# Performance work log

Hardware: AMD Instinct MI355X
Metric: run time of the kernel (lower is better)

## Reference

```python
import jax, jax.numpy as jnp
import numpy as np

HEADS = 8
DIM_HEAD = 96
INNER = HEADS * DIM_HEAD  # 768
PEP_DIM = 768
PRO_DIM = 768
SCALE = DIM_HEAD ** -0.5
NEG = -1000000.0
EPS = 1e-5


def _layer_norm(x, g, b):
    mu = jnp.mean(x, axis=-1, keepdims=True)
    var = jnp.mean(jnp.square(x - mu), axis=-1, keepdims=True)
    return (x - mu) * jax.lax.rsqrt(var + EPS) * g + b


def setup_inputs() -> dict:
    key = jax.random.key(0)
    ks = jax.random.split(key, 12)
    b, n, m = 16, 128, 2048
    peptide = jax.random.normal(ks[0], (b, n, PEP_DIM), dtype=jnp.float32)
    protein = jax.random.normal(ks[1], (b, m, PRO_DIM), dtype=jnp.float32)
    peptide_mask = jax.random.randint(ks[2], (b, n), 0, 2, dtype=jnp.int32)
    pro_mask = jax.random.randint(ks[3], (b, m), 0, 2, dtype=jnp.int32)
    s = 0.02
    Wq = jax.random.normal(ks[4], (PEP_DIM, INNER), dtype=jnp.float32) * s
    Wk = jax.random.normal(ks[5], (PRO_DIM, INNER), dtype=jnp.float32) * s
    Wv_prot = jax.random.normal(ks[6], (PRO_DIM, INNER), dtype=jnp.float32) * s
    Wv_pep = jax.random.normal(ks[7], (PEP_DIM, INNER), dtype=jnp.float32) * s
    Wo_prot = jax.random.normal(ks[8], (INNER, PEP_DIM), dtype=jnp.float32) * s
    bo_prot = jnp.zeros((PEP_DIM,), dtype=jnp.float32)
    Wo_pep = jax.random.normal(ks[9], (INNER, PRO_DIM), dtype=jnp.float32) * s
    bo_pep = jnp.zeros((PRO_DIM,), dtype=jnp.float32)
    ln_g = jnp.ones((PEP_DIM,), dtype=jnp.float32)
    ln_b = jnp.zeros((PEP_DIM,), dtype=jnp.float32)
    return {
        'peptide': peptide, 'protein': protein,
        'peptide_mask': peptide_mask, 'pro_mask': pro_mask,
        'Wq': Wq, 'Wk': Wk, 'Wv_prot': Wv_prot, 'Wv_pep': Wv_pep,
        'Wo_prot': Wo_prot, 'bo_prot': bo_prot,
        'Wo_pep': Wo_pep, 'bo_pep': bo_pep,
        'ln_g': ln_g, 'ln_b': ln_b,
    }


def reference(peptide, protein, peptide_mask, pro_mask,
              Wq, Wk, Wv_prot, Wv_pep, Wo_prot, bo_prot, Wo_pep, bo_pep,
              ln_g, ln_b):
    b, n, _ = peptide.shape
    m = protein.shape[1]
    # projections -> (b, h, len, d)
    q = (peptide @ Wq).reshape(b, n, HEADS, DIM_HEAD).transpose(0, 2, 1, 3)
    k = (protein @ Wk).reshape(b, m, HEADS, DIM_HEAD).transpose(0, 2, 1, 3)
    v_prot = (protein @ Wv_prot).reshape(b, m, HEADS, DIM_HEAD).transpose(0, 2, 1, 3)
    v_pep = (peptide @ Wv_pep).reshape(b, n, HEADS, DIM_HEAD).transpose(0, 2, 1, 3)
    # scores (b, h, n, m)
    dots = jnp.einsum('bhnd,bhmd->bhnm', q, k) * SCALE
    dots = jnp.where(peptide_mask[:, None, :, None] == 0, NEG, dots)
    dots = jnp.where(pro_mask[:, None, None, :] == 0, NEG, dots)
    attn = jax.nn.softmax(dots, axis=-1)
    # peptide-side output: rows of attn aggregate protein values
    out_protein = jnp.einsum('bhnm,bhmd->bhnd', attn, v_prot)
    out_protein = out_protein.transpose(0, 2, 1, 3).reshape(b, n, INNER)
    out_protein = out_protein @ Wo_prot + bo_prot
    out_protein = _layer_norm(out_protein + peptide, ln_g, ln_b)
    # protein-side output: attn^T aggregates peptide values
    out_peptide = jnp.einsum('bhnm,bhnd->bhmd', attn, v_pep)
    out_peptide = out_peptide.transpose(0, 2, 1, 3).reshape(b, m, INNER)
    out_peptide = out_peptide @ Wo_pep + bo_pep
    out_peptide = _layer_norm(out_peptide + protein, ln_g, ln_b)
    return (out_protein, out_peptide, attn)
```

## Files before the change

### kernel.cpp

```cpp
#include <hip/hip_runtime.h>
#include <math.h>

static constexpr int HEADS  = 8;
static constexpr int DHEAD  = 96;
static constexpr int INNER  = 768;
static constexpr int NPEP   = 128;
static constexpr int MPRO   = 2048;
static constexpr float ATT_SCALE = 0.10206207261596577f;
static constexpr float NEGF   = -1000000.0f;
static constexpr float LN_EPS = 1e-5f;

typedef __attribute__((ext_vector_type(8))) short bf16x8;
typedef __attribute__((ext_vector_type(4))) float f32x4;

__device__ __forceinline__ unsigned short f2b(float f) {
    unsigned u = __builtin_bit_cast(unsigned, f);
    u += 0x7fffu + ((u >> 16) & 1u);
    return (unsigned short)(u >> 16);
}
__device__ __forceinline__ float b2f(unsigned short u) {
    return __builtin_bit_cast(float, (unsigned)u << 16);
}

__device__ __forceinline__ void async16(const unsigned short* g, unsigned short* l) {
    __builtin_amdgcn_global_load_lds(
        (const __attribute__((address_space(1))) void*)g,
        (__attribute__((address_space(3))) void*)l, 16, 0, 0);
}

template<int TM, int MODE>
__global__ __launch_bounds__(256) void gemm_bf16(
    const unsigned short* __restrict__ A, const unsigned short* __restrict__ B,
    unsigned short* __restrict__ C,
    int M, int N, int K, int lda, int ldb, int ldc,
    long sAb, long sAh, long sBb, long sBh, long sCb, long sCh,
    int lenShift, int nxSwz,
    const unsigned short* __restrict__ B2, unsigned short* __restrict__ C2)
{
    (void)M;
    constexpr int FR   = TM / 32;
    constexpr int PIPE = 3;
    __shared__ unsigned short As[PIPE][TM * 32];
    __shared__ unsigned short Bs[PIPE][128 * 32];

    const int tid = threadIdx.x;
    int bx, by;
    if (nxSwz > 0) {
        const int bid = blockIdx.x;
        const int per = gridDim.x >> 3;
        const int v   = (bid & 7) * per + (bid >> 3);
        bx = v % nxSwz; by = v / nxSwz;
    } else { bx = blockIdx.x; by = blockIdx.y; }
    int n0        = bx * 128;
    const int m0  = by * TM;
    const int z   = blockIdx.z;
    const int zb  = z >> 3, zh = z & 7;

    bool sideB = false;
    if (MODE == 5 && n0 >= 768) { sideB = true; n0 -= 768; }

    const unsigned short* Ab = A + zb * sAb + zh * sAh;
    const unsigned short* Bb = ((MODE == 5 && sideB) ? B2 : B) + zb * sBb + zh * sBh;

    const int rS = tid >> 2;
    const int kS = (((tid & 3) ^ ((rS >> 1) & 3)) * 8);
    const int wave = tid >> 6;

    const int lane = tid & 63;
    const int l16  = lane & 15;
    const int quad = lane >> 4;
    const int wr   = (wave >> 1) * (TM / 2);
    const int wc   = (wave & 1) * 64;

    f32x4 acc[FR][4];
#pragma unroll
    for (int i = 0; i < FR; ++i)
#pragma unroll
        for (int j = 0; j < 4; ++j) acc[i][j] = (f32x4){0.f, 0.f, 0.f, 0.f};

    auto stageT = [&](int t, int bi) {
        const int k0 = t << 5;
        unsigned short* a0 = &As[bi][wave * 512];
        async16(Ab + (long)(m0 + rS) * lda + k0 + kS, a0);
        if (TM == 128)
            async16(Ab + (long)(m0 + 64 + rS) * lda + k0 + kS, a0 + 2048);
        int bR0 = n0 + rS;      if (bR0 > N - 1) bR0 = N - 1;
        int bR1 = n0 + 64 + rS; if (bR1 > N - 1) bR1 = N - 1;
        unsigned short* b0 = &Bs[bi][wave * 512];
        async16(Bb + (long)bR0 * ldb + k0 + kS, b0);
        async16(Bb + (long)bR1 * ldb + k0 + kS, b0 + 2048);
    };

    const int NT = K >> 5;
    stageT(0, 0);
    if (NT > 1) stageT(1, 1);
    if (NT > 2) stageT(2, 2);

    int bi = 0;
    for (int t = 0; t < NT; ++t) {
        const int ahead = NT - 1 - t;
        if constexpr (TM == 128) {
            if (ahead >= 2)      asm volatile("s_waitcnt vmcnt(8)" ::: "memory");
            else if (ahead == 1) asm volatile("s_waitcnt vmcnt(4)" ::: "memory");
            else                 asm volatile("s_waitcnt vmcnt(0)" ::: "memory");
        } else {
            if (ahead >= 2)      asm volatile("s_waitcnt vmcnt(6)" ::: "memory");
            else if (ahead == 1) asm volatile("s_waitcnt vmcnt(3)" ::: "memory");
            else                 asm volatile("s_waitcnt vmcnt(0)" ::: "memory");
        }
        __builtin_amdgcn_s_barrier();

        bf16x8 af[FR], bfr[4];
#pragma unroll
        for (int i = 0; i < FR; ++i) {
            const int rA = wr + i * 16 + l16;
            af[i] = *reinterpret_cast<const bf16x8*>(
                &As[bi][rA * 32 + ((quad ^ ((rA >> 1) & 3)) * 8)]);
        }
#pragma unroll
        for (int j = 0; j < 4; ++j) {
            const int rB = wc + j * 16 + l16;
            bfr[j] = *reinterpret_cast<const bf16x8*>(
                &Bs[bi][rB * 32 + ((quad ^ ((rB >> 1) & 3)) * 8)]);
        }

        __builtin_amdgcn_s_setprio(1);
#pragma unroll
        for (int i = 0; i < FR; ++i)
#pragma unroll
            for (int j = 0; j < 4; ++j)
                acc[i][j] = __builtin_amdgcn_mfma_f32_16x16x32_bf16(af[i], bfr[j], acc[i][j], 0, 0, 0);
        __builtin_amdgcn_s_setprio(0);

        __builtin_amdgcn_s_barrier();
        __builtin_amdgcn_sched_barrier(0);
        if (t + PIPE < NT) stageT(t + PIPE, bi);
        bi = bi + 1; if (bi == PIPE) bi = 0;
    }

#pragma unroll
    for (int i = 0; i < FR; ++i) {
#pragma unroll
        for (int j = 0; j < 4; ++j) {
            const int col = n0 + wc + j * 16 + l16;
            if ((MODE == 2) && col >= N) continue;
            const int h = col / 96, d = col - h * 96;
#pragma unroll
            for (int r = 0; r < 4; ++r) {
                const int row = m0 + wr + i * 16 + quad * 4 + r;
                float v = acc[i][j][r];
                if (MODE == 1) {
                    v *= ATT_SCALE;
                    C[zb * sCb + zh * sCh + (long)row * ldc + col] = f2b(v);
                } else if (MODE == 2) {
                    C[zb * sCb + zh * sCh + (long)row * ldc + col] = f2b(v);
                } else if (MODE == 3) {
                    const int bb = row >> lenShift, rr = row & ((1 << lenShift) - 1);
                    C[(((long)(bb * 8 + h) << lenShift) + rr) * 96 + d] = f2b(v);
                } else if (MODE == 4) {
                    const int bb = row >> lenShift, rr = row & ((1 << lenShift) - 1);
                    C[(((long)(bb * 8 + h) * 96 + d) << lenShift) + rr] = f2b(v);
                } else {
                    const int bb = row >> lenShift, rr = row & ((1 << lenShift) - 1);
                    if (!sideB)
                        C [(((long)(bb * 8 + h) << lenShift) + rr) * 96 + d] = f2b(v);
                    else
                        C2[(((long)(bb * 8 + h) * 96 + d) << lenShift) + rr] = f2b(v);
                }
            }
        }
    }
}

__global__ __launch_bounds__(256) void fusedpv_kernel(
    const unsigned short* __restrict__ attn16,
    const unsigned short* __restrict__ vprotT,
    const unsigned short* __restrict__ vpepT,
    unsigned short* __restrict__ opp,
    unsigned short* __restrict__ opep)
{
    __shared__ unsigned short AttT[128 * 136];
    __shared__ unsigned short Vp[96 * 136];

    const int id = blockIdx.x;
    const int z  = ((id >> 4) << 3) + (id & 7);
    const int nh = (id >> 3) & 1;
    const int b  = z >> 3, h = z & 7;

    const unsigned short* Az = attn16 + (long)z * NPEP * MPRO;
    const unsigned short* Vz = vprotT + (long)z * 96 * MPRO;
    const unsigned short* Pz = vpepT  + (long)z * 96 * 128;

    const int tid  = threadIdx.x;
    const int lane = tid & 63;
    const int l16  = lane & 15;
    const int quad = lane >> 4;
    const int wave = tid >> 6;
    const int wrN  = (wave >> 1) * 32;
    const int wrM  = (wave >> 1) * 64;
    const int wcD  = (wave & 1) * 48;

#pragma unroll
    for (int e = 0; e < 6; ++e) {
        const int c = tid + e * 256;
        const int row = c >> 4, coloff = (c & 15) * 8;
        bf16x8 v = *reinterpret_cast<const bf16x8*>(Pz + row * 128 + coloff);
        *reinterpret_cast<bf16x8*>(&Vp[row * 136 + coloff]) = v;
    }
    __syncthreads();

    f32x4 acc1[2][3];
#pragma unroll
    for (int i = 0; i < 2; ++i)
#pragma unroll
        for (int j = 0; j < 3; ++j) acc1[i][j] = (f32x4){0.f, 0.f, 0.f, 0.f};

    for (int cc = 0; cc < 16; ++cc) {
        const int m0 = cc * 128;
        const bool own = (cc >> 3) == nh;

        bf16x8 a1[2][4], b1[3][4];
#pragma unroll
        for (int i = 0; i < 2; ++i) {
            const int n = nh * 64 + wrN + i * 16 + l16;
#pragma unroll
            for (int kc = 0; kc < 4; ++kc)
                a1[i][kc] = *reinterpret_cast<const bf16x8*>(
                    Az + (long)n * MPRO + m0 + kc * 32 + quad * 8);
        }
#pragma unroll
        for (int j = 0; j < 3; ++j) {
            const int d = wcD + j * 16 + l16;
#pragma unroll
            for (int kc = 0; kc < 4; ++kc)
                b1[j][kc] = *reinterpret_cast<const bf16x8*>(
                    Vz + (long)d * MPRO + m0 + kc * 32 + quad * 8);
        }

        if (own) {
            const int mBase = (tid & 7) * 16;
#pragma unroll
            for (int nn = 0; nn < 128; nn += 32) {
                const int n = nn + (tid >> 3);
#pragma unroll
                for (int c = 0; c < 2; ++c) {
                    bf16x8 v = *reinterpret_cast<const bf16x8*>(
                        Az + (long)n * MPRO + m0 + mBase + c * 8);
#pragma unroll
                    for (int jj = 0; jj < 8; ++jj)
                        AttT[(mBase + c * 8 + jj) * 136 + n] = (unsigned short)v[jj];
                }
            }
            __syncthreads();
        }

#pragma unroll
        for (int kc = 0; kc < 4; ++kc)
#pragma unroll
            for (int i = 0; i < 2; ++i)
#pragma unroll
                for (int j = 0; j < 3; ++j)
                    acc1[i][j] = __builtin_amdgcn_mfma_f32_16x16x32_bf16(
                        a1[i][kc], b1[j][kc], acc1[i][j], 0, 0, 0);

        if (own) {
            f32x4 acc2[4][3];
#pragma unroll
            for (int i = 0; i < 4; ++i)
#pragma unroll
                for (int j = 0; j < 3; ++j) acc2[i][j] = (f32x4){0.f, 0.f, 0.f, 0.f};
#pragma unroll
            for (int kc = 0; kc < 4; ++kc) {
                bf16x8 a2[4], b2v[3];
#pragma unroll
                for (int i = 0; i < 4; ++i)
                    a2[i] = *reinterpret_cast<const bf16x8*>(
                        &AttT[(wrM + i * 16 + l16) * 136 + kc * 32 + quad * 8]);
#pragma unroll
                for (int j = 0; j < 3; ++j)
                    b2v[j] = *reinterpret_cast<const bf16x8*>(
                        &Vp[(wcD + j * 16 + l16) * 136 + kc * 32 + quad * 8]);
#pragma unroll
                for (int i = 0; i < 4; ++i)
#pragma unroll
                    for (int j = 0; j < 3; ++j)
                        acc2[i][j] = __builtin_amdgcn_mfma_f32_16x16x32_bf16(
                            a2[i], b2v[j], acc2[i][j], 0, 0, 0);
            }
#pragma unroll
            for (int i = 0; i < 4; ++i)
#pragma unroll
                for (int j = 0; j < 3; ++j) {
                    const int d = wcD + j * 16 + l16;
#pragma unroll
                    for (int r = 0; r < 4; ++r) {
                        const int m = m0 + wrM + i * 16 + quad * 4 + r;
                        opep[(long)b * MPRO * INNER + (long)m * INNER + h * 96 + d]
                            = f2b(acc2[i][j][r]);
                    }
                }
            __syncthreads();
        }
    }

#pragma unroll
    for (int i = 0; i < 2; ++i)
#pragma unroll
        for (int j = 0; j < 3; ++j) {
            const int d = wcD + j * 16 + l16;
#pragma unroll
            for (int r = 0; r < 4; ++r) {
                const int n = nh * 64 + wrN + i * 16 + quad * 4 + r;
                opp[((long)b * NPEP + n) * INNER + h * 96 + d] = f2b(acc1[i][j][r]);
            }
        }
}

__global__ __launch_bounds__(256) void conv2_kernel(
    const float* __restrict__ pro, const float* __restrict__ pep,
    unsigned short* __restrict__ pro16, unsigned short* __restrict__ pep16,
    int nPro4, int nPep4)
{
    const int i = blockIdx.x * 256 + threadIdx.x;
    const float* in; unsigned short* out; int idx;
    if (i < nPro4) { in = pro; out = pro16; idx = i; }
    else { idx = i - nPro4; if (idx >= nPep4) return; in = pep; out = pep16; }
    float4 v = reinterpret_cast<const float4*>(in)[idx];
    ushort4 o;
    o.x = f2b(v.x); o.y = f2b(v.y); o.z = f2b(v.z); o.w = f2b(v.w);
    reinterpret_cast<ushort4*>(out)[idx] = o;
}

__global__ __launch_bounds__(256) void wtrans_kernel(
    const float* w0, const float* w1, const float* w2,
    const float* w3, const float* w4, const float* w5,
    unsigned short* o0, unsigned short* o1, unsigned short* o2,
    unsigned short* o3, unsigned short* o4, unsigned short* o5)
{
    const float* in; unsigned short* out;
    switch (blockIdx.z) {
        case 0: in = w0; out = o0; break;
        case 1: in = w1; out = o1; break;
        case 2: in = w2; out = o2; break;
        case 3: in = w3; out = o3; break;
        case 4: in = w4; out = o4; break;
        default: in = w5; out = o5; break;
    }
    __shared__ unsigned short t[32][33];
    const int bx = blockIdx.x * 32, by = blockIdx.y * 32;
    const int x = threadIdx.x, y = threadIdx.y;
#pragma unroll
    for (int i = 0; i < 32; i += 8)
        t[y + i][x] = f2b(in[(long)(by + y + i) * 768 + bx + x]);
    __syncthreads();
#pragma unroll
    for (int i = 0; i < 32; i += 8)
        out[(long)(bx + y + i) * 768 + by + x] = t[x][y + i];
}

__global__ __launch_bounds__(256) void softmax_kernel(
    unsigned short* __restrict__ s16, float* __restrict__ attn,
    const int* __restrict__ pepm, const int* __restrict__ prom)
{
    __shared__ float smx[4], sms[4];
    const long row = blockIdx.x;
    const int b = (int)(row >> 10);
    const int n = (int)(row & 127);
    unsigned short* p16 = s16 + row * (long)MPRO;
    float* pf = attn + row * (long)MPRO;
    const int tid = threadIdx.x;
    const int wv = tid >> 6;
    const int rowOk = pepm[(b << 7) + n];

    float v[8];
    float mx = -3.4e38f;
    if (rowOk) {
#pragma unroll
        for (int k = 0; k < 8; ++k) {
            const int c = tid + k * 256;
            float x = b2f(p16[c]);
            if (prom[(b << 11) + c] == 0) x = NEGF;
            v[k] = x; mx = fmaxf(mx, x);
        }
    } else {
#pragma unroll
        for (int k = 0; k < 8; ++k) v[k] = NEGF;
        mx = NEGF;
    }
#pragma unroll
    for (int off = 32; off > 0; off >>= 1) mx = fmaxf(mx, __shfl_xor(mx, off));
    if ((tid & 63) == 0) smx[wv] = mx;
    __syncthreads();
    mx = fmaxf(fmaxf(smx[0], smx[1]), fmaxf(smx[2], smx[3]));

    float sum = 0.f;
#pragma unroll
    for (int k = 0; k < 8; ++k) { v[k] = __expf(v[k] - mx); sum += v[k]; }
#pragma unroll
    for (int off = 32; off > 0; off >>= 1) sum += __shfl_xor(sum, off);
    if ((tid & 63) == 0) sms[wv] = sum;
    __syncthreads();
    const float inv = 1.0f / (sms[0] + sms[1] + sms[2] + sms[3]);
#pragma unroll
    for (int k = 0; k < 8; ++k) {
        const float o = v[k] * inv;
        pf[tid + k * 256] = o;
        p16[tid + k * 256] = f2b(o);
    }
}

__global__ __launch_bounds__(256) void bias_res_ln(
    const unsigned short* __restrict__ tmp, const float* __restrict__ bias,
    const float* __restrict__ res, const float* __restrict__ gam,
    const float* __restrict__ bet, float* __restrict__ out)
{
    __shared__ float red[8];
    const long row = blockIdx.x;
    const unsigned short* t = tmp + row * INNER;
    const float* r = res + row * INNER;
    float* o = out + row * INNER;
    const int tid = threadIdx.x;
    const int wv = tid >> 6;

    float v[3]; float s = 0.f;
#pragma unroll
    for (int k = 0; k < 3; ++k) { const int c = tid + k * 256; v[k] = b2f(t[c]) + bias[c] + r[c]; s += v[k]; }
#pragma unroll
    for (int off = 32; off > 0; off >>= 1) s += __shfl_xor(s, off);
    if ((tid & 63) == 0) red[wv] = s;
    __syncthreads();
    const float mu = (red[0] + red[1] + red[2] + red[3]) * (1.0f / INNER);

    float vs = 0.f;
#pragma unroll
    for (int k = 0; k < 3; ++k) { const float d = v[k] - mu; vs += d * d; }
#pragma unroll
    for (int off = 32; off > 0; off >>= 1) vs += __shfl_xor(vs, off);
    if ((tid & 63) == 0) red[4 + wv] = vs;
    __syncthreads();
    const float rstd = rsqrtf((red[4] + red[5] + red[6] + red[7]) * (1.0f / INNER) + LN_EPS);
#pragma unroll
    for (int k = 0; k < 3; ++k) { const int c = tid + k * 256; o[c] = (v[k] - mu) * rstd * gam[c] + bet[c]; }
}

extern "C" void kernel_launch(void* const* d_in, const int* in_sizes, int n_in,
                              void* d_out, int out_size, void* d_ws, size_t ws_size,
                              hipStream_t stream)
{
    (void)in_sizes; (void)n_in; (void)out_size; (void)ws_size;

    const float* peptide = (const float*)d_in[0];
    const float* protein = (const float*)d_in[1];
    const int*   pepm    = (const int*)  d_in[2];
    const int*   prom    = (const int*)  d_in[3];
    const float* Wq      = (const float*)d_in[4];
    const float* Wk      = (const float*)d_in[5];
    const float* Wv_prot = (const float*)d_in[6];
    const float* Wv_pep  = (const float*)d_in[7];
    const float* Wo_prot = (const float*)d_in[8];
    const float* bo_prot = (const float*)d_in[9];
    const float* Wo_pep  = (const float*)d_in[10];
    const float* bo_pep  = (const float*)d_in[11];
    const float* ln_g    = (const float*)d_in[12];
    const float* ln_b    = (const float*)d_in[13];

    char* ws = (char*)d_ws;
    auto U = [&](size_t off) { return (unsigned short*)(ws + off); };
    unsigned short* WT0   = U(0);
    unsigned short* WT1   = U(1179648);
    unsigned short* WT2   = U(2 * 1179648);
    unsigned short* WT3   = U(3 * 1179648);
    unsigned short* WT4   = U(4 * 1179648);
    unsigned short* WT5   = U(5 * 1179648);
    unsigned short* q16   = U(7077888);
    unsigned short* k16   = U(10223616);
    unsigned short* vpT   = U(60555264);
    unsigned short* vpepT = U(110886912);
    unsigned short* s16   = U(114032640);
    unsigned short* pro16 = U(114032640);
    unsigned short* pep16 = U(164364288);
    unsigned short* opp   = U(7077888);
    unsigned short* opep  = U(10223616);
    unsigned short* tmp1  = U(164364288);
    unsigned short* tmp2  = U(63700992);

    float* outP = (float*)d_out;
    float* outQ = outP + 16 * 128 * 768;
    float* attn = outQ + (long)16 * 2048 * 768;

    conv2_kernel<<<26112, 256, 0, stream>>>(protein, peptide, pro16, pep16, 6291456, 393216);
    wtrans_kernel<<<dim3(24, 24, 6), dim3(32, 8), 0, stream>>>(
        Wq, Wk, Wv_prot, Wv_pep, Wo_prot, Wo_pep, WT0, WT1, WT2, WT3, WT4, WT5);

    gemm_bf16<128, 5><<<dim3(12, 16, 1), 256, 0, stream>>>(
        pep16, WT0, q16, 2048, 768, 768, 768, 768, 0,
        0, 0, 0, 0, 0, 0, 7, 0, WT3, vpepT);
    gemm_bf16<128, 5><<<dim3(3072, 1, 1), 256, 0, stream>>>(
        pro16, WT1, k16, 32768, 768, 768, 768, 768, 0,
        0, 0, 0, 0, 0, 0, 11, 12, WT2, vpT);

    gemm_bf16<128, 1><<<dim3(16, 1, 128), 256, 0, stream>>>(
        q16, k16, s16, 128, 2048, 96, 96, 96, 2048,
        98304L, 12288L, 1572864L, 196608L, 2097152L, 262144L, 0, 0, nullptr, nullptr);

    softmax_kernel<<<16384, 256, 0, stream>>>(s16, attn, pepm, prom);

    fusedpv_kernel<<<256, 256, 0, stream>>>(s16, vpT, vpepT, opp, opep);

    gemm_bf16<64, 2><<<dim3(6, 32, 1), 256, 0, stream>>>(
        opp, WT4, tmp1, 2048, 768, 768, 768, 768, 768,
        0, 0, 0, 0, 0, 0, 0, 0, nullptr, nullptr);
    bias_res_ln<<<2048, 256, 0, stream>>>(tmp1, bo_prot, peptide, ln_g, ln_b, outP);

    gemm_bf16<128, 2><<<dim3(1536, 1, 1), 256, 0, stream>>>(
        opep, WT5, tmp2, 32768, 768, 768, 768, 768, 768,
        0, 0, 0, 0, 0, 0, 0, 6, nullptr, nullptr);
    bias_res_ln<<<32768, 256, 0, stream>>>(tmp2, bo_pep, protein, ln_g, ln_b, outQ);
}
```

Before: 746.6 us.

## Use 256x256-tile 512-thread GEMM for large protein projections

After: 774.3 us. +3.7%, slower.

```diff
diff --git a/kernel.cpp b/kernel.cpp
--- a/kernel.cpp
+++ b/kernel.cpp
@@ -26,6 +26,119 @@
     __builtin_amdgcn_global_load_lds(
         (const __attribute__((address_space(1))) void*)g,
         (__attribute__((address_space(3))) void*)l, 16, 0, 0);
+}
+
+template<int MODE>
+__global__ __launch_bounds__(512) void gemm256(
+    const unsigned short* __restrict__ A, const unsigned short* __restrict__ B,
+    unsigned short* __restrict__ C,
+    int N, int K, int lda, int ldb, int ldc,
+    int lenShift, int nx,
+    const unsigned short* __restrict__ B2, unsigned short* __restrict__ C2)
+{
+    __shared__ unsigned short As[2][256 * 32];
+    __shared__ unsigned short Bs[2][256 * 32];
+
+    const int tid = threadIdx.x;
+    const int bid = blockIdx.x;
+    const int per = gridDim.x >> 3;
+    const int v   = (bid & 7) * per + (bid >> 3);
+    int n0        = (v % nx) * 256;
+    const int m0  = (v / nx) * 256;
+
+    bool sideB = false;
+    if (MODE == 5 && n0 >= 768) { sideB = true; n0 -= 768; }
+
+    const unsigned short* Bb = (MODE == 5 && sideB) ? B2 : B;
+
+    const int rS = tid >> 2;
+    const int kS = (((tid & 3) ^ ((rS >> 1) & 3)) * 8);
+    const int wave = tid >> 6;
+
+    const int lane = tid & 63;
+    const int l16  = lane & 15;
+    const int quad = lane >> 4;
+    const int wr   = (wave >> 2) * 128;
+    const int wc   = (wave & 3) * 64;
+
+    f32x4 acc[8][4];
+#pragma unroll
+    for (int i = 0; i < 8; ++i)
+#pragma unroll
+        for (int j = 0; j < 4; ++j) acc[i][j] = (f32x4){0.f, 0.f, 0.f, 0.f};
+
+    auto stageT = [&](int t, int bi) {
+        const int k0 = t << 5;
+        unsigned short* a0 = &As[bi][wave * 512];
+        async16(A + (long)(m0 + rS) * lda + k0 + kS, a0);
+        async16(A + (long)(m0 + 128 + rS) * lda + k0 + kS, a0 + 4096);
+        int bR0 = n0 + rS;       if (bR0 > N - 1) bR0 = N - 1;
+        int bR1 = n0 + 128 + rS; if (bR1 > N - 1) bR1 = N - 1;
+        unsigned short* b0 = &Bs[bi][wave * 512];
+        async16(Bb + (long)bR0 * ldb + k0 + kS, b0);
+        async16(Bb + (long)bR1 * ldb + k0 + kS, b0 + 4096);
+    };
+
+    const int NT = K >> 5;
+    stageT(0, 0);
+    stageT(1, 1);
+
+    for (int t = 0; t < NT; ++t) {
+        const int bi = t & 1;
+        if (t < NT - 1) asm volatile("s_waitcnt vmcnt(4)" ::: "memory");
+        else            asm volatile("s_waitcnt vmcnt(0)" ::: "memory");
+        __builtin_amdgcn_s_barrier();
+
+        bf16x8 af[8], bfr[4];
+#pragma unroll
+        for (int j = 0; j < 4; ++j) {
+            const int rB = wc + j * 16 + l16;
+            bfr[j] = *reinterpret_cast<const bf16x8*>(
+                &Bs[bi][rB * 32 + ((quad ^ ((rB >> 1) & 3)) * 8)]);
+        }
+#pragma unroll
+        for (int i = 0; i < 8; ++i) {
+            const int rA = wr + i * 16 + l16;
+            af[i] = *reinterpret_cast<const bf16x8*>(
+                &As[bi][rA * 32 + ((quad ^ ((rA >> 1) & 3)) * 8)]);
+        }
+
+        __builtin_amdgcn_s_setprio(1);
+#pragma unroll
+        for (int i = 0; i < 8; ++i)
+#pragma unroll
+            for (int j = 0; j < 4; ++j)
+                acc[i][j] = __builtin_amdgcn_mfma_f32_16x16x32_bf16(af[i], bfr[j], acc[i][j], 0, 0, 0);
+        __builtin_amdgcn_s_setprio(0);
+
+        __builtin_amdgcn_s_barrier();
+        __builtin_amdgcn_sched_barrier(0);
+        if (t + 2 < NT) stageT(t + 2, bi);
+    }
+
+#pragma unroll
+    for (int i = 0; i < 8; ++i) {
+#pragma unroll
+        for (int j = 0; j < 4; ++j) {
+            const int col = n0 + wc + j * 16 + l16;
+            if ((MODE == 2) && col >= N) continue;
+            const int h = col / 96, d = col - h * 96;
+#pragma unroll
+            for (int r = 0; r < 4; ++r) {
+                const int row = m0 + wr + i * 16 + quad * 4 + r;
+                float val = acc[i][j][r];
+                if (MODE == 2) {
+                    C[(long)row * ldc + col] = f2b(val);
+                } else {
+                    const int bb = row >> lenShift, rr = row & ((1 << lenShift) - 1);
+                    if (!sideB)
+                        C [(((long)(bb * 8 + h) << lenShift) + rr) * 96 + d] = f2b(val);
+                    else
+                        C2[(((long)(bb * 8 + h) * 96 + d) << lenShift) + rr] = f2b(val);
+                }
+            }
+        }
+    }
 }
 
 template<int TM, int MODE>
@@ -495,9 +608,9 @@
     gemm_bf16<128, 5><<<dim3(12, 16, 1), 256, 0, stream>>>(
         pep16, WT0, q16, 2048, 768, 768, 768, 768, 0,
         0, 0, 0, 0, 0, 0, 7, 0, WT3, vpepT);
-    gemm_bf16<128, 5><<<dim3(3072, 1, 1), 256, 0, stream>>>(
-        pro16, WT1, k16, 32768, 768, 768, 768, 768, 0,
-        0, 0, 0, 0, 0, 0, 11, 12, WT2, vpT);
+    gemm256<5><<<768, 512, 0, stream>>>(
+        pro16, WT1, k16, 768, 768, 768, 768, 0,
+        11, 6, WT2, vpT);
 
     gemm_bf16<128, 1><<<dim3(16, 1, 128), 256, 0, stream>>>(
         q16, k16, s16, 128, 2048, 96, 96, 96, 2048,
@@ -512,8 +625,8 @@
         0, 0, 0, 0, 0, 0, 0, 0, nullptr, nullptr);
     bias_res_ln<<<2048, 256, 0, stream>>>(tmp1, bo_prot, peptide, ln_g, ln_b, outP);
 
-    gemm_bf16<128, 2><<<dim3(1536, 1, 1), 256, 0, stream>>>(
-        opep, WT5, tmp2, 32768, 768, 768, 768, 768, 768,
-        0, 0, 0, 0, 0, 0, 0, 6, nullptr, nullptr);
+    gemm256<2><<<384, 512, 0, stream>>>(
+        opep, WT5, tmp2, 768, 768, 768, 768, 768,
+        0, 3, nullptr, nullptr);
     bias_res_ln<<<32768, 256, 0, stream>>>(tmp2, bo_pep, protein, ln_g, ln_b, outQ);
 }
```
